# Performance work log

Measured on AMD Instinct MI355X. Metric: run time of the kernel, lower is better.

Reference implementation:

```python
import math
import jax, jax.numpy as jnp
import numpy as np

B, S, DM = 2, 1024, 1024
H, D = 16, 64
BUCKETS, MAX_POS = 256, 512
SPAN = BUCKETS          # pos_ebd_size = position_buckets
SCALE = math.sqrt(D * 3)  # scale_factor = 1 + len([c2p, p2c])
EPS = 1e-7


def _make_log_bucket_position(rel, bucket_size, max_position):
    # numpy, matches make_log_bucket_position exactly (static, shape-derived)
    sign = np.sign(rel)
    mid = bucket_size // 2
    abs_pos = np.where((rel < mid) & (rel > -mid), mid - 1, np.abs(rel))
    log_pos = np.ceil(np.log(abs_pos / mid) / np.log((max_position - 1) / mid) * (mid - 1)) + mid
    return np.where(abs_pos <= mid, rel, (log_pos * sign)).astype(np.int64)


def _build_relative_position(q_size, k_size):
    rel = np.arange(q_size)[:, None] - np.arange(k_size)[None, :]
    return _make_log_bucket_position(rel, BUCKETS, MAX_POS)  # [q, k]


def setup_inputs() -> dict:
    key = jax.random.key(0)
    ks = jax.random.split(key, 12)
    w = lambda k, sh: (jax.random.normal(k, sh, jnp.float32) * 0.02)
    return {
        "hidden_states": jax.random.normal(ks[0], (B, S, DM), jnp.float32),
        "rel_embeddings": jax.random.normal(ks[1], (2 * SPAN, DM), jnp.float32),
        "Wq": w(ks[2], (DM, DM)), "bq": jnp.zeros((DM,), jnp.float32),
        "Wk": w(ks[3], (DM, DM)), "bk": jnp.zeros((DM,), jnp.float32),
        "Wv": w(ks[4], (DM, DM)), "bv": jnp.zeros((DM,), jnp.float32),
        "Wo": w(ks[5], (DM, DM)), "bo": jnp.zeros((DM,), jnp.float32),
        "ln_w": jnp.ones((DM,), jnp.float32), "ln_b": jnp.zeros((DM,), jnp.float32),
        "attention_mask": jnp.ones((B, 1, S, S), jnp.int32),
    }


def reference(hidden_states, rel_embeddings, Wq, bq, Wk, bk, Wv, bv, Wo, bo, ln_w, ln_b, attention_mask):
    b, s, _ = hidden_states.shape
    heads = lambda x: x.reshape(b, s, H, D).transpose(0, 2, 1, 3)  # [B,H,S,D]
    q = heads(hidden_states @ Wq + bq)
    k = heads(hidden_states @ Wk + bk)
    v = heads(hidden_states @ Wv + bv)

    # content-to-content scores
    scores = jnp.einsum('bhqd,bhkd->bhqk', q, k) / SCALE

    # disentangled relative-position bias (share_att_key=True: reuse key/query proj)
    rel = _build_relative_position(s, s)                      # [S,S] static int
    c2p_idx = np.clip(rel + SPAN, 0, 2 * SPAN - 1)            # [S,S]
    p2c_idx = np.clip(-rel + SPAN, 0, 2 * SPAN - 1)           # [S,S]
    pos_k = (rel_embeddings @ Wk + bk).reshape(2 * SPAN, H, D).transpose(1, 0, 2)  # [H,P,D]
    pos_q = (rel_embeddings @ Wq + bq).reshape(2 * SPAN, H, D).transpose(1, 0, 2)  # [H,P,D]

    qi = np.arange(s)[:, None]  # row index for gather along bucket axis
    c2p = jnp.einsum('bhqd,hpd->bhqp', q, pos_k)              # [B,H,S,2K]
    scores = scores + c2p[:, :, qi, c2p_idx] / SCALE          # gather -> [B,H,S,S]
    p2c = jnp.einsum('bhkd,hpd->bhkp', k, pos_q)              # [B,H,S,2K]
    scores = scores + jnp.swapaxes(p2c[:, :, qi, p2c_idx], -1, -2) / SCALE

    # XSoftmax: masked softmax, masked positions zeroed
    m = attention_mask.astype(bool)
    probs = jax.nn.softmax(jnp.where(m, scores, -jnp.inf), axis=-1)
    probs = jnp.where(m, probs, 0.0)

    ctx = jnp.einsum('bhqk,bhkd->bhqd', probs, v).transpose(0, 2, 1, 3).reshape(b, s, H * D)

    # DebertaV2SelfOutput: dense + (eval-mode dropout = identity) + LayerNorm residual
    h = ctx @ Wo + bo + hidden_states
    mu = h.mean(-1, keepdims=True)
    var = ((h - mu) ** 2).mean(-1, keepdims=True)
    return (h - mu) * jax.lax.rsqrt(var + EPS) * ln_w + ln_b
```

## Files before the change

### kernel.cpp

```cpp
#include <hip/hip_runtime.h>
#include <hip/hip_bf16.h>

#define Sv   1024
#define DMv  1024
#define Hv   16
#define PBv  512
#define INVSCALE 0.07216878364870322f

typedef unsigned short u16;
typedef unsigned int   u32;
typedef short  short8  __attribute__((ext_vector_type(8)));
typedef float  float4v __attribute__((ext_vector_type(4)));

__device__ __forceinline__ float b2f(u16 u) {
    union { u32 u; float f; } c; c.u = ((u32)u) << 16; return c.f;
}
__device__ __forceinline__ u16 f2b(float f) {
    union { float f; u32 u; } c; c.f = f;
    u32 u = c.u;
    return (u16)((u + 0x7fffu + ((u >> 16) & 1u)) >> 16);
}
__device__ __forceinline__ float ldE(const void* p, size_t i, bool f32) {
    return f32 ? ((const float*)p)[i] : b2f(((const u16*)p)[i]);
}

__device__ __forceinline__ void gld16(const u16* g, u16* l) {
    __builtin_amdgcn_global_load_lds(
        (const __attribute__((address_space(1))) void*)g,
        (__attribute__((address_space(3))) void*)l,
        16, 0, 0);
}

__global__ void setup_kernel(const u32* __restrict__ w, int* __restrict__ flag,
                             int* __restrict__ tbl) {
    if (blockIdx.x == 0) {
        int t = threadIdx.x;
        if (t < 64) {
            int c = 0;
            #pragma unroll
            for (int i = 0; i < 4; i++) {
                u32 v = w[t * 4 + i];
                c += (((v >> 23) & 0xFFu) < 0x80u) ? 1 : 0;
            }
            #pragma unroll
            for (int off = 32; off > 0; off >>= 1) c += __shfl_down(c, off, 64);
            if (t == 0) *flag = (c > 128) ? 1 : 0;
        }
        return;
    }
    int i = (blockIdx.x - 1) * 256 + threadIdx.x;
    if (i >= 2047) return;
    int rel = i - 1023;
    const int mid = 128;
    int abs_pos = (rel < mid && rel > -mid) ? (mid - 1) : (rel < 0 ? -rel : rel);
    int bucket;
    if (abs_pos <= mid) {
        bucket = rel;
    } else {
        double lp = ceil(log((double)abs_pos / 128.0) / log(511.0 / 128.0) * 127.0) + 128.0;
        bucket = (int)lp * (rel > 0 ? 1 : -1);
    }
    int idx = bucket + 256;
    idx = idx < 0 ? 0 : (idx > 511 ? 511 : idx);
    tbl[i] = idx;
}

__global__ __launch_bounds__(256) void cvt2_kernel(
    const void* __restrict__ s0, u16* __restrict__ d0,
    const void* __restrict__ s1, u16* __restrict__ d1,
    const int* __restrict__ flagp)
{
    bool f32 = (*flagp != 0);
    const void* src; u16* dst; size_t i;
    if (blockIdx.x < 1024) {
        src = s0; dst = d0;
        i = ((size_t)blockIdx.x * 256 + threadIdx.x) * 8;
    } else {
        src = s1; dst = d1;
        i = ((size_t)(blockIdx.x - 1024) * 256 + threadIdx.x) * 8;
    }
    if (f32) {
        const float* s = (const float*)src + i;
        float4 a = *(const float4*)s;
        float4 b = *(const float4*)(s + 4);
        uint4 o = make_uint4(f2b(a.x) | (f2b(a.y) << 16), f2b(a.z) | (f2b(a.w) << 16),
                             f2b(b.x) | (f2b(b.y) << 16), f2b(b.z) | (f2b(b.w) << 16));
        *(uint4*)(dst + i) = o;
    } else {
        *(uint4*)(dst + i) = *(const uint4*)((const u16*)src + i);
    }
}

__global__ __launch_bounds__(256) void transpose_cvt(
    const void* __restrict__ S0, const void* __restrict__ S1,
    const void* __restrict__ S2, u16* __restrict__ out,
    const int* __restrict__ flagp)
{
    bool f32 = (*flagp != 0);
    int z = blockIdx.z;
    const void* S = (z == 0) ? S0 : (z == 1) ? S1 : S2;
    u16* O = out + (size_t)z * 1048576;
    int k0 = blockIdx.x * 64, n0 = blockIdx.y * 64;
    __shared__ u16 Ls[64][72];
    int t = threadIdx.x;
    int r = t >> 2, cseg = (t & 3) * 16;

    u16 v[16];
    size_t base = (size_t)(k0 + r) * 1024 + n0 + cseg;
    if (f32) {
        const float* p = (const float*)S + base;
        #pragma unroll
        for (int i = 0; i < 16; i += 4) {
            float4 f = *(const float4*)(p + i);
            v[i] = f2b(f.x); v[i + 1] = f2b(f.y); v[i + 2] = f2b(f.z); v[i + 3] = f2b(f.w);
        }
    } else {
        const u16* p = (const u16*)S + base;
        uint4 a = *(const uint4*)p, b = *(const uint4*)(p + 8);
        u32 wd[8] = {a.x, a.y, a.z, a.w, b.x, b.y, b.z, b.w};
        #pragma unroll
        for (int i = 0; i < 8; i++) { v[2 * i] = (u16)(wd[i] & 0xffff); v[2 * i + 1] = (u16)(wd[i] >> 16); }
    }
    #pragma unroll
    for (int i = 0; i < 16; i++) Ls[cseg + i][r] = v[i];
    __syncthreads();

    int n = t >> 2, kseg = (t & 3) * 16;
    u16* op = O + (size_t)(n0 + n) * 1024 + k0 + kseg;
    *(uint4*)op       = *(const uint4*)&Ls[n][kseg];
    *(uint4*)(op + 8) = *(const uint4*)&Ls[n][kseg + 8];
}

__global__ __launch_bounds__(256) void wgemm_bt(
    const u16* __restrict__ A,
    const u16* __restrict__ B0, const u16* __restrict__ B1, const u16* __restrict__ B2,
    const void* __restrict__ b0, const void* __restrict__ b1, const void* __restrict__ b2,
    u16* __restrict__ O0, u16* __restrict__ O1, u16* __restrict__ O2,
    const int* __restrict__ flagp, int vseg, int sseg)
{
    bool f32 = (*flagp != 0);
    __shared__ u16 As[128][64];
    __shared__ u16 Bs[128][64];

    int t = threadIdx.x;
    int seg = blockIdx.x >> 3;
    int n0  = (blockIdx.x & 7) * 128;
    int m0  = blockIdx.y * 128;
    const u16* Bt = (seg == 0) ? B0 : (seg == 1) ? B1 : B2;
    const void* bi = (seg == 0) ? b0 : (seg == 1) ? b1 : b2;
    u16* O = (seg == 0) ? O0 : (seg == 1) ? O1 : O2;
    float es = (seg == sseg) ? INVSCALE : 1.0f;

    int w = t >> 6, lane = t & 63;
    int quad = lane >> 4, l16 = lane & 15;
    int wm = (w >> 1) * 64, wn = (w & 1) * 64;

    float4v acc[4][4];
    #pragma unroll
    for (int i = 0; i < 4; i++)
        #pragma unroll
        for (int j = 0; j < 4; j++)
            acc[i][j] = (float4v){0.f, 0.f, 0.f, 0.f};

    int lr8  = lane >> 3;
    int lcol = (lane & 7) * 8;
    const u16* ap0 = A  + (size_t)(m0 + w * 32 + lr8) * 1024 + lcol;
    const u16* bp0 = Bt + (size_t)(n0 + w * 32 + lr8) * 1024 + lcol;

    for (int k0 = 0; k0 < 1024; k0 += 64) {
        __syncthreads();
        #pragma unroll
        for (int i = 0; i < 4; i++) {
            gld16(ap0 + (size_t)(i * 8) * 1024 + k0, &As[w * 32 + i * 8][0]);
            gld16(bp0 + (size_t)(i * 8) * 1024 + k0, &Bs[w * 32 + i * 8][0]);
        }
        __syncthreads();

        #pragma unroll
        for (int kk = 0; kk < 64; kk += 32) {
            short8 af[4], bf[4];
            #pragma unroll
            for (int i = 0; i < 4; i++)
                af[i] = *(const short8*)&As[wm + i * 16 + l16][kk + quad * 8];
            #pragma unroll
            for (int j = 0; j < 4; j++)
                bf[j] = *(const short8*)&Bs[wn + j * 16 + l16][kk + quad * 8];
            #pragma unroll
            for (int j = 0; j < 4; j++)
                #pragma unroll
                for (int i = 0; i < 4; i++)
                    acc[i][j] = __builtin_amdgcn_mfma_f32_16x16x32_bf16(af[i], bf[j], acc[i][j], 0, 0, 0);
        }
    }

    if (seg == vseg) {
        #pragma unroll
        for (int j = 0; j < 4; j++) {
            int ncol = n0 + wn + j * 16 + l16;
            float bv = ldE(bi, ncol, f32);
            u16* obase = O + (size_t)(ncol >> 6) * 131072 + (size_t)(ncol & 63) * 2048;
            #pragma unroll
            for (int i = 0; i < 4; i++) {
                int rbase = m0 + wm + i * 16 + quad * 4;
                u32 w0 = (u32)f2b((acc[i][j][0] + bv) * es) | ((u32)f2b((acc[i][j][1] + bv) * es) << 16);
                u32 w1 = (u32)f2b((acc[i][j][2] + bv) * es) | ((u32)f2b((acc[i][j][3] + bv) * es) << 16);
                *(uint2*)(obase + rbase) = make_uint2(w0, w1);
            }
        }
    } else {
        #pragma unroll
        for (int j = 0; j < 4; j++) {
            int ncol = n0 + wn + j * 16 + l16;
            float bv = ldE(bi, ncol, f32);
            #pragma unroll
            for (int i = 0; i < 4; i++) {
                int rbase = m0 + wm + i * 16 + quad * 4;
                #pragma unroll
                for (int r = 0; r < 4; r++)
                    O[(size_t)(rbase + r) * 1024 + ncol] = f2b((acc[i][j][r] + bv) * es);
            }
        }
    }
}

__global__ __launch_bounds__(256) void wgemm_bt_m64(
    const u16* __restrict__ A, const u16* __restrict__ Bt,
    const void* __restrict__ bi, u16* __restrict__ O,
    const int* __restrict__ flagp)
{
    bool f32 = (*flagp != 0);
    __shared__ u16 As[64][64];
    __shared__ u16 Bs[128][64];

    int t = threadIdx.x;
    int n0 = blockIdx.x * 128;
    int m0 = blockIdx.y * 64;

    int w = t >> 6, lane = t & 63;
    int quad = lane >> 4, l16 = lane & 15;
    int wm = (w >> 1) * 32, wn = (w & 1) * 64;

    float4v acc[2][4];
    #pragma unroll
    for (int i = 0; i < 2; i++)
        #pragma unroll
        for (int j = 0; j < 4; j++)
            acc[i][j] = (float4v){0.f, 0.f, 0.f, 0.f};

    int lr8  = lane >> 3;
    int lcol = (lane & 7) * 8;
    const u16* ap0 = A  + (size_t)(m0 + w * 16 + lr8) * 1024 + lcol;
    const u16* bp0 = Bt + (size_t)(n0 + w * 32 + lr8) * 1024 + lcol;

    for (int k0 = 0; k0 < 1024; k0 += 64) {
        __syncthreads();
        #pragma unroll
        for (int i = 0; i < 2; i++)
            gld16(ap0 + (size_t)(i * 8) * 1024 + k0, &As[w * 16 + i * 8][0]);
        #pragma unroll
        for (int i = 0; i < 4; i++)
            gld16(bp0 + (size_t)(i * 8) * 1024 + k0, &Bs[w * 32 + i * 8][0]);
        __syncthreads();

        #pragma unroll
        for (int kk = 0; kk < 64; kk += 32) {
            short8 af[2], bf[4];
            #pragma unroll
            for (int i = 0; i < 2; i++)
                af[i] = *(const short8*)&As[wm + i * 16 + l16][kk + quad * 8];
            #pragma unroll
            for (int j = 0; j < 4; j++)
                bf[j] = *(const short8*)&Bs[wn + j * 16 + l16][kk + quad * 8];
            #pragma unroll
            for (int j = 0; j < 4; j++)
                #pragma unroll
                for (int i = 0; i < 2; i++)
                    acc[i][j] = __builtin_amdgcn_mfma_f32_16x16x32_bf16(af[i], bf[j], acc[i][j], 0, 0, 0);
        }
    }

    #pragma unroll
    for (int j = 0; j < 4; j++) {
        int ncol = n0 + wn + j * 16 + l16;
        float bv = ldE(bi, ncol, f32);
        #pragma unroll
        for (int i = 0; i < 2; i++) {
            int rbase = m0 + wm + i * 16 + quad * 4;
            #pragma unroll
            for (int r = 0; r < 4; r++)
                O[(size_t)(rbase + r) * 1024 + ncol] = f2b(acc[i][j][r] + bv);
        }
    }
}

__global__ __launch_bounds__(256) void pos_score_mfma(
    const u16* __restrict__ Xq, const u16* __restrict__ Xk,
    const u16* __restrict__ PK, const u16* __restrict__ PQ,
    u16* __restrict__ outq, u16* __restrict__ outk)
{
    int zT = blockIdx.z;
    const u16* X = zT ? Xk : Xq;
    const u16* P = zT ? PQ : PK;
    u16* out     = zT ? outk : outq;

    __shared__ u16 As[128][64];
    __shared__ u16 Bs[128][64];
    int t = threadIdx.x;
    int h  = blockIdx.x >> 2;
    int j0 = (blockIdx.x & 3) * 128;
    int m0 = blockIdx.y * 128;

    int w = t >> 6, lane = t & 63;
    int quad = lane >> 4, l16 = lane & 15;
    int wm = (w >> 1) * 64, wn = (w & 1) * 64;

    int lr8  = lane >> 3;
    int lcol = (lane & 7) * 8;
    {
        const u16* xp = X + (size_t)(m0 + w * 32 + lr8) * 1024 + h * 64 + lcol;
        const u16* pp = P + (size_t)(j0 + w * 32 + lr8) * 1024 + h * 64 + lcol;
        #pragma unroll
        for (int i = 0; i < 4; i++) {
            gld16(xp + (size_t)(i * 8) * 1024, &As[w * 32 + i * 8][0]);
            gld16(pp + (size_t)(i * 8) * 1024, &Bs[w * 32 + i * 8][0]);
        }
    }
    __syncthreads();

    float4v acc[4][4];
    #pragma unroll
    for (int i = 0; i < 4; i++)
        #pragma unroll
        for (int j = 0; j < 4; j++)
            acc[i][j] = (float4v){0.f, 0.f, 0.f, 0.f};

    #pragma unroll
    for (int k0 = 0; k0 < 64; k0 += 32) {
        short8 af[4], bf[4];
        #pragma unroll
        for (int i = 0; i < 4; i++)
            af[i] = *(const short8*)&As[wm + i * 16 + l16][k0 + quad * 8];
        #pragma unroll
        for (int j = 0; j < 4; j++)
            bf[j] = *(const short8*)&Bs[wn + j * 16 + l16][k0 + quad * 8];
        #pragma unroll
        for (int j = 0; j < 4; j++)
            #pragma unroll
            for (int i = 0; i < 4; i++)
                acc[i][j] = __builtin_amdgcn_mfma_f32_16x16x32_bf16(af[i], bf[j], acc[i][j], 0, 0, 0);
    }

    if (zT == 0) {
        #pragma unroll
        for (int j = 0; j < 4; j++) {
            int jc = j0 + wn + j * 16 + l16;
            #pragma unroll
            for (int i = 0; i < 4; i++) {
                int rbase = m0 + wm + i * 16 + quad * 4;
                #pragma unroll
                for (int r = 0; r < 4; r++)
                    out[((size_t)h * Sv + rbase + r) * PBv + jc] = f2b(acc[i][j][r]);
            }
        }
    } else {
        #pragma unroll
        for (int j = 0; j < 4; j++) {
            int jc = j0 + wn + j * 16 + l16;
            u16* obase = out + (size_t)h * (PBv * Sv) + (size_t)jc * Sv;
            #pragma unroll
            for (int i = 0; i < 4; i++) {
                int rbase = m0 + wm + i * 16 + quad * 4;
                u32 w0 = (u32)f2b(acc[i][j][0]) | ((u32)f2b(acc[i][j][1]) << 16);
                u32 w1 = (u32)f2b(acc[i][j][2]) | ((u32)f2b(acc[i][j][3]) << 16);
                *(uint2*)(obase + rbase) = make_uint2(w0, w1);
            }
        }
    }
}

__global__ __launch_bounds__(256, 2) void attn6_kernel(
    const u16* __restrict__ Q, const u16* __restrict__ K,
    const u16* __restrict__ Vtg,
    const u16* __restrict__ C2P,
    const u16* __restrict__ P2Ct,
    const int* __restrict__ tbl, u16* __restrict__ CTX)
{
    __shared__ u16 Qc[32][72];
    __shared__ u16 Kc[2][64][72];
    __shared__ u16 Vc[2][64][72];
    __shared__ u16 Pb[4][16][72];
    __shared__ short stbl[2047];
    __shared__ float msh[2][2][16], lsh[2][2][16];

    int t = threadIdx.x, w = t >> 6, lane = t & 63;
    int qg = w >> 1, ks = w & 1;
    int quad = lane >> 4, l16 = lane & 15;
    int h = blockIdx.y, q0 = blockIdx.x * 32;

    for (int i = t; i < 2047; i += 256) stbl[i] = (short)tbl[i];
    {
        int row = t >> 3, dseg = (t & 7) * 8;
        *(uint4*)&Qc[row][dseg] =
            *(const uint4*)(Q + (size_t)(q0 + row) * DMv + h * 64 + dseg);
    }
    __syncthreads();

    short8 afq0 = *(const short8*)&Qc[qg * 16 + l16][quad * 8];
    short8 afq1 = *(const short8*)&Qc[qg * 16 + l16][quad * 8 + 32];

    int qrow = q0 + qg * 16 + quad * 4;
    const u16* c2p_h  = C2P  + (size_t)h * (Sv * PBv);
    const u16* p2ct_h = P2Ct + (size_t)h * (PBv * Sv);
    const u16* vt_h   = Vtg  + (size_t)h * 131072;

    float m[4] = {-1e30f, -1e30f, -1e30f, -1e30f};
    float l[4] = {0.f, 0.f, 0.f, 0.f};
    float4v Ov[4];
    #pragma unroll
    for (int j = 0; j < 4; j++) Ov[j] = (float4v){0.f, 0.f, 0.f, 0.f};

    int srow = (t >> 1) & 63, sseg = (t & 1) * 32, ssp = t >> 7;

    for (int c = 0; c < 8; c++) {
        __syncthreads();
        {
            int kglob = ssp * 512 + c * 64 + srow;
            const u16* kp = K + (size_t)kglob * DMv + h * 64 + sseg;
            uint4 a0 = *(const uint4*)(kp + 0);
            uint4 a1 = *(const uint4*)(kp + 8);
            uint4 a2 = *(const uint4*)(kp + 16);
            uint4 a3 = *(const uint4*)(kp + 24);
            *(uint4*)&Kc[ssp][srow][sseg + 0]  = a0;
            *(uint4*)&Kc[ssp][srow][sseg + 8]  = a1;
            *(uint4*)&Kc[ssp][srow][sseg + 16] = a2;
            *(uint4*)&Kc[ssp][srow][sseg + 24] = a3;
            const u16* vp = vt_h + (size_t)srow * 2048 + ssp * 512 + c * 64 + sseg;
            uint4 v0 = *(const uint4*)(vp + 0);
            uint4 v1 = *(const uint4*)(vp + 8);
            uint4 v2 = *(const uint4*)(vp + 16);
            uint4 v3 = *(const uint4*)(vp + 24);
            *(uint4*)&Vc[ssp][srow][sseg + 0]  = v0;
            *(uint4*)&Vc[ssp][srow][sseg + 8]  = v1;
            *(uint4*)&Vc[ssp][srow][sseg + 16] = v2;
            *(uint4*)&Vc[ssp][srow][sseg + 24] = v3;
        }
        __syncthreads();

        int kb = ks * 512 + c * 64;
        float p[4][4];
        #pragma unroll
        for (int j = 0; j < 4; j++) {
            short8 bk0 = *(const short8*)&Kc[ks][j * 16 + l16][quad * 8];
            short8 bk1 = *(const short8*)&Kc[ks][j * 16 + l16][quad * 8 + 32];
            float4v a = (float4v){0.f, 0.f, 0.f, 0.f};
            a = __builtin_amdgcn_mfma_f32_16x16x32_bf16(afq0, bk0, a, 0, 0, 0);
            a = __builtin_amdgcn_mfma_f32_16x16x32_bf16(afq1, bk1, a, 0, 0, 0);
            #pragma unroll
            for (int r = 0; r < 4; r++) p[j][r] = a[r];
        }
        #pragma unroll
        for (int j = 0; j < 4; j++) {
            int k = kb + j * 16 + l16;
            #pragma unroll
            for (int r = 0; r < 4; r++) {
                int q = qrow + r;
                int idx = stbl[q - k + 1023];
                p[j][r] = p[j][r] + b2f(c2p_h[(size_t)q * PBv + idx])
                                  + b2f(p2ct_h[(size_t)idx * Sv + k]);
            }
        }
        float corr[4];
        #pragma unroll
        for (int r = 0; r < 4; r++) {
            float v = fmaxf(fmaxf(p[0][r], p[1][r]), fmaxf(p[2][r], p[3][r]));
            v = fmaxf(v, __shfl_xor(v, 1, 64));
            v = fmaxf(v, __shfl_xor(v, 2, 64));
            v = fmaxf(v, __shfl_xor(v, 4, 64));
            v = fmaxf(v, __shfl_xor(v, 8, 64));
            float nm = fmaxf(m[r], v);
            corr[r] = __expf(m[r] - nm);
            m[r] = nm;
        }
        #pragma unroll
        for (int r = 0; r < 4; r++) {
            #pragma unroll
            for (int j = 0; j < 4; j++) p[j][r] = __expf(p[j][r] - m[r]);
            float s = p[0][r] + p[1][r] + p[2][r] + p[3][r];
            s += __shfl_xor(s, 1, 64);
            s += __shfl_xor(s, 2, 64);
            s += __shfl_xor(s, 4, 64);
            s += __shfl_xor(s, 8, 64);
            l[r] = l[r] * corr[r] + s;
            #pragma unroll
            for (int j = 0; j < 4; j++) Ov[j][r] *= corr[r];
        }
        #pragma unroll
        for (int j = 0; j < 4; j++)
            #pragma unroll
            for (int r = 0; r < 4; r++)
                Pb[w][quad * 4 + r][j * 16 + l16] = f2b(p[j][r]);
        short8 ap0 = *(const short8*)&Pb[w][l16][quad * 8];
        short8 ap1 = *(const short8*)&Pb[w][l16][quad * 8 + 32];
        #pragma unroll
        for (int j = 0; j < 4; j++) {
            short8 bv0 = *(const short8*)&Vc[ks][j * 16 + l16][quad * 8];
            short8 bv1 = *(const short8*)&Vc[ks][j * 16 + l16][quad * 8 + 32];
            Ov[j] = __builtin_amdgcn_mfma_f32_16x16x32_bf16(ap0, bv0, Ov[j], 0, 0, 0);
            Ov[j] = __builtin_amdgcn_mfma_f32_16x16x32_bf16(ap1, bv1, Ov[j], 0, 0, 0);
        }
    }

    if (l16 == 0) {
        #pragma unroll
        for (int r = 0; r < 4; r++) {
            msh[qg][ks][quad * 4 + r] = m[r];
            lsh[qg][ks][quad * 4 + r] = l[r];
        }
    }
    __syncthreads();
    float scl[4];
    #pragma unroll
    for (int r = 0; r < 4; r++) {
        int row = quad * 4 + r;
        float m0 = msh[qg][0][row], m1 = msh[qg][1][row];
        float M = fmaxf(m0, m1);
        float L = lsh[qg][0][row] * __expf(m0 - M) + lsh[qg][1][row] * __expf(m1 - M);
        scl[r] = __expf(m[r] - M) / L;
    }
    float* Obuf = (float*)&Kc[0][0][0];
    if (ks == 1) {
        #pragma unroll
        for (int j = 0; j < 4; j++)
            #pragma unroll
            for (int r = 0; r < 4; r++)
                Obuf[(qg * 16 + quad * 4 + r) * 66 + j * 16 + l16] = Ov[j][r] * scl[r];
    }
    __syncthreads();
    if (ks == 0) {
        #pragma unroll
        for (int j = 0; j < 4; j++)
            #pragma unroll
            for (int r = 0; r < 4; r++) {
                float v = Ov[j][r] * scl[r]
                        + Obuf[(qg * 16 + quad * 4 + r) * 66 + j * 16 + l16];
                CTX[(size_t)(qrow + r) * DMv + h * 64 + j * 16 + l16] = f2b(v);
            }
    }
}

__global__ __launch_bounds__(256) void ln_kernel(
    const u16* __restrict__ Hb, const void* __restrict__ hidden,
    const void* __restrict__ lnw, const void* __restrict__ lnb,
    void* __restrict__ out, const int* __restrict__ flagp)
{
    bool f32 = (*flagp != 0);
    int row = blockIdx.x;
    int t = threadIdx.x;
    const u16* hp = Hb + (size_t)row * DMv;

    uint2 hv = *(const uint2*)(hp + t * 4);
    float x[4];
    x[0] = b2f(hv.x & 0xffff); x[1] = b2f(hv.x >> 16);
    x[2] = b2f(hv.y & 0xffff); x[3] = b2f(hv.y >> 16);
    size_t rb = (size_t)row * DMv + t * 4;
    if (f32) {
        float4 xv = *(const float4*)((const float*)hidden + rb);
        x[0] += xv.x; x[1] += xv.y; x[2] += xv.z; x[3] += xv.w;
    } else {
        uint2 xv = *(const uint2*)((const u16*)hidden + rb);
        x[0] += b2f(xv.x & 0xffff); x[1] += b2f(xv.x >> 16);
        x[2] += b2f(xv.y & 0xffff); x[3] += b2f(xv.y >> 16);
    }

    float s1 = x[0] + x[1] + x[2] + x[3];
    float s2 = x[0] * x[0] + x[1] * x[1] + x[2] * x[2] + x[3] * x[3];
    #pragma unroll
    for (int off = 32; off > 0; off >>= 1) {
        s1 += __shfl_down(s1, off, 64);
        s2 += __shfl_down(s2, off, 64);
    }
    __shared__ float r1[4], r2[4];
    int wave = t >> 6, lane = t & 63;
    if (lane == 0) { r1[wave] = s1; r2[wave] = s2; }
    __syncthreads();
    float ts1 = r1[0] + r1[1] + r1[2] + r1[3];
    float ts2 = r2[0] + r2[1] + r2[2] + r2[3];
    float mu  = ts1 * (1.0f / DMv);
    float var = fmaxf(ts2 * (1.0f / DMv) - mu * mu, 0.f);
    float rs  = rsqrtf(var + 1e-7f);
    #pragma unroll
    for (int i = 0; i < 4; i++) {
        int c = t * 4 + i;
        float v = (x[i] - mu) * rs * ldE(lnw, c, f32) + ldE(lnb, c, f32);
        if (f32) ((float*)out)[(size_t)row * DMv + c] = v;
        else     ((u16*)out)[(size_t)row * DMv + c] = f2b(v);
    }
}

extern "C" void kernel_launch(void* const* d_in, const int* in_sizes, int n_in,
                              void* d_out, int out_size, void* d_ws, size_t ws_size,
                              hipStream_t stream) {
    const void* hidden = d_in[0];
    const void* rel    = d_in[1];
    const void* Wq = d_in[2];  const void* bq = d_in[3];
    const void* Wk = d_in[4];  const void* bk = d_in[5];
    const void* Wv = d_in[6];  const void* bv = d_in[7];
    const void* Wo = d_in[8];  const void* bo = d_in[9];
    const void* lnw = d_in[10]; const void* lnb = d_in[11];

    const size_t MB = 1u << 20;
    char* ws = (char*)d_ws;
    int* FLAG = (int*)ws;
    int* TBL  = (int*)(ws + 1024);
    char* base = ws + (64 << 10);
    u16* Qb   = (u16*)(base + 0 * MB);
    u16* Kb   = (u16*)(base + 4 * MB);
    u16* Vt   = (u16*)(base + 8 * MB);
    u16* CTX  = (u16*)(base + 12 * MB);
    u16* Xb   = (u16*)(base + 12 * MB);
    u16* PKb  = (u16*)(base + 16 * MB);
    u16* PQb  = (u16*)(base + 17 * MB);
    u16* HB   = (u16*)(base + 16 * MB);
    u16* C2P  = (u16*)(base + 18 * MB);
    u16* WoT  = (u16*)(base + 20 * MB);
    u16* P2Ct = (u16*)(base + 34 * MB);
    u16* WqT  = (u16*)(base + 34 * MB);
    u16* WkT  = (u16*)(base + 36 * MB);
    u16* WvT  = (u16*)(base + 38 * MB);
    u16* relb = (u16*)(base + 40 * MB);

    dim3 blk(256);

    setup_kernel<<<9, blk, 0, stream>>>((const u32*)Wq, FLAG, TBL);
    cvt2_kernel<<<1280, blk, 0, stream>>>(hidden, Xb, rel, relb, FLAG);
    transpose_cvt<<<dim3(16, 16, 3), blk, 0, stream>>>(Wq, Wk, Wv, WqT, FLAG);

    wgemm_bt<<<dim3(24, 16), blk, 0, stream>>>(
        Xb, WqT, WkT, WvT, bq, bk, bv, Qb, Kb, Vt, FLAG, 2, 0);
    wgemm_bt<<<dim3(16, 4), blk, 0, stream>>>(
        relb, WkT, WqT, nullptr, bk, bq, nullptr, PKb, PQb, nullptr, FLAG, -1, 1);

    for (int b = 0; b < 2; b++) {
        size_t off = (size_t)b * Sv * DMv;
        pos_score_mfma<<<dim3(64, 8, 2), blk, 0, stream>>>(
            Qb + off, Kb + off, PKb, PQb, C2P, P2Ct);
        attn6_kernel<<<dim3(32, 16), blk, 0, stream>>>(
            Qb + off, Kb + off, Vt + (size_t)b * 1024, C2P, P2Ct, TBL, CTX + off);
    }

    transpose_cvt<<<dim3(16, 16, 1), blk, 0, stream>>>(Wo, nullptr, nullptr, WoT, FLAG);
    wgemm_bt_m64<<<dim3(8, 32), blk, 0, stream>>>(CTX, WoT, bo, HB, FLAG);
    ln_kernel<<<2048, blk, 0, stream>>>(HB, hidden, lnw, lnb, d_out, FLAG);
}
```

Measured before the change: 286.6 us.

## Transpose p2c GEMM operands for coalesced stores; alias Qc/Pb LDS for higher occupancy

For the p2c half, the pos-score kernel now swaps the GEMM operands: it computes PQ x Xk directly, so the result lands in the transposed [P,S] layout with row-contiguous scalar stores instead of packed strided column writes. Both branches now share one store loop. The attention kernel places Qc and Pb in a shared-memory union, which is safe because Qc is read into registers before Pb is first written. It also raises launch bounds from 2 to 3 blocks per SM to increase occupancy, at the risk of register pressure or spills.

```diff
diff --git a/kernel.cpp b/kernel.cpp
--- a/kernel.cpp
+++ b/kernel.cpp
@@ -299,16 +299,18 @@
     u16* __restrict__ outq, u16* __restrict__ outk)
 {
     int zT = blockIdx.z;
-    const u16* X = zT ? Xk : Xq;
-    const u16* P = zT ? PQ : PK;
-    u16* out     = zT ? outk : outq;
+    int h  = blockIdx.x >> 2;
+    int a  = blockIdx.x & 3;
+    int m0 = zT ? a * 128 : blockIdx.y * 128;
+    int n0 = zT ? blockIdx.y * 128 : a * 128;
+    const u16* Am = zT ? PQ : Xq;
+    const u16* Bn = zT ? Xk : PK;
+    u16* out      = zT ? outk : outq;
+    size_t cs     = zT ? (size_t)Sv : (size_t)PBv;
 
     __shared__ u16 As[128][64];
     __shared__ u16 Bs[128][64];
     int t = threadIdx.x;
-    int h  = blockIdx.x >> 2;
-    int j0 = (blockIdx.x & 3) * 128;
-    int m0 = blockIdx.y * 128;
 
     int w = t >> 6, lane = t & 63;
     int quad = lane >> 4, l16 = lane & 15;
@@ -317,8 +319,8 @@
     int lr8  = lane >> 3;
     int lcol = (lane & 7) * 8;
     {
-        const u16* xp = X + (size_t)(m0 + w * 32 + lr8) * 1024 + h * 64 + lcol;
-        const u16* pp = P + (size_t)(j0 + w * 32 + lr8) * 1024 + h * 64 + lcol;
+        const u16* xp = Am + (size_t)(m0 + w * 32 + lr8) * 1024 + h * 64 + lcol;
+        const u16* pp = Bn + (size_t)(n0 + w * 32 + lr8) * 1024 + h * 64 + lcol;
         #pragma unroll
         for (int i = 0; i < 4; i++) {
             gld16(xp + (size_t)(i * 8) * 1024, &As[w * 32 + i * 8][0]);
@@ -350,45 +352,33 @@
                 acc[i][j] = __builtin_amdgcn_mfma_f32_16x16x32_bf16(af[i], bf[j], acc[i][j], 0, 0, 0);
     }
 
-    if (zT == 0) {
-        #pragma unroll
-        for (int j = 0; j < 4; j++) {
-            int jc = j0 + wn + j * 16 + l16;
-            #pragma unroll
-            for (int i = 0; i < 4; i++) {
-                int rbase = m0 + wm + i * 16 + quad * 4;
-                #pragma unroll
-                for (int r = 0; r < 4; r++)
-                    out[((size_t)h * Sv + rbase + r) * PBv + jc] = f2b(acc[i][j][r]);
-            }
-        }
-    } else {
-        #pragma unroll
-        for (int j = 0; j < 4; j++) {
-            int jc = j0 + wn + j * 16 + l16;
-            u16* obase = out + (size_t)h * (PBv * Sv) + (size_t)jc * Sv;
-            #pragma unroll
-            for (int i = 0; i < 4; i++) {
-                int rbase = m0 + wm + i * 16 + quad * 4;
-                u32 w0 = (u32)f2b(acc[i][j][0]) | ((u32)f2b(acc[i][j][1]) << 16);
-                u32 w1 = (u32)f2b(acc[i][j][2]) | ((u32)f2b(acc[i][j][3]) << 16);
-                *(uint2*)(obase + rbase) = make_uint2(w0, w1);
-            }
-        }
-    }
-}
-
-__global__ __launch_bounds__(256, 2) void attn6_kernel(
+    u16* oh = out + (size_t)h * ((size_t)PBv * Sv);
+    #pragma unroll
+    for (int j = 0; j < 4; j++) {
+        int jc = n0 + wn + j * 16 + l16;
+        #pragma unroll
+        for (int i = 0; i < 4; i++) {
+            int rbase = m0 + wm + i * 16 + quad * 4;
+            #pragma unroll
+            for (int r = 0; r < 4; r++)
+                oh[(size_t)(rbase + r) * cs + jc] = f2b(acc[i][j][r]);
+        }
+    }
+}
+
+__global__ __launch_bounds__(256, 3) void attn6_kernel(
     const u16* __restrict__ Q, const u16* __restrict__ K,
     const u16* __restrict__ Vtg,
     const u16* __restrict__ C2P,
     const u16* __restrict__ P2Ct,
     const int* __restrict__ tbl, u16* __restrict__ CTX)
 {
-    __shared__ u16 Qc[32][72];
+    __shared__ union {
+        u16 Qc[32][72];
+        u16 Pb[4][16][72];
+    } QP;
     __shared__ u16 Kc[2][64][72];
     __shared__ u16 Vc[2][64][72];
-    __shared__ u16 Pb[4][16][72];
     __shared__ short stbl[2047];
     __shared__ float msh[2][2][16], lsh[2][2][16];
 
@@ -400,13 +390,13 @@
     for (int i = t; i < 2047; i += 256) stbl[i] = (short)tbl[i];
     {
         int row = t >> 3, dseg = (t & 7) * 8;
-        *(uint4*)&Qc[row][dseg] =
+        *(uint4*)&QP.Qc[row][dseg] =
             *(const uint4*)(Q + (size_t)(q0 + row) * DMv + h * 64 + dseg);
     }
     __syncthreads();
 
-    short8 afq0 = *(const short8*)&Qc[qg * 16 + l16][quad * 8];
-    short8 afq1 = *(const short8*)&Qc[qg * 16 + l16][quad * 8 + 32];
+    short8 afq0 = *(const short8*)&QP.Qc[qg * 16 + l16][quad * 8];
+    short8 afq1 = *(const short8*)&QP.Qc[qg * 16 + l16][quad * 8 + 32];
 
     int qrow = q0 + qg * 16 + quad * 4;
     const u16* c2p_h  = C2P  + (size_t)h * (Sv * PBv);
@@ -498,9 +488,9 @@
         for (int j = 0; j < 4; j++)
             #pragma unroll
             for (int r = 0; r < 4; r++)
-                Pb[w][quad * 4 + r][j * 16 + l16] = f2b(p[j][r]);
-        short8 ap0 = *(const short8*)&Pb[w][l16][quad * 8];
-        short8 ap1 = *(const short8*)&Pb[w][l16][quad * 8 + 32];
+                QP.Pb[w][quad * 4 + r][j * 16 + l16] = f2b(p[j][r]);
+        short8 ap0 = *(const short8*)&QP.Pb[w][l16][quad * 8];
+        short8 ap1 = *(const short8*)&QP.Pb[w][l16][quad * 8 + 32];
         #pragma unroll
         for (int j = 0; j < 4; j++) {
             short8 bv0 = *(const short8*)&Vc[ks][j * 16 + l16][quad * 8];
```

Measured after the change: 342.7 us. 19.6% more time.
